# Optimization experiments

Hardware: AMD Instinct MI355X
Metric: run time of the kernel (lower is better)

Reference implementation:

```python
import jax, jax.numpy as jnp
from jax import lax
import numpy as np

GAMMA = 0.25  # bottleneck commitment-loss weight (bn.gamma)
B, Q, N = 8, 64, 8192
K = 512       # n_quant_vecs (codebook size)
C = 256       # n_classes (mu-law quantization levels)


def setup_inputs() -> dict:
    key = jax.random.key(0)
    k1, k2, k3, k4 = jax.random.split(key, 4)
    ze = jax.random.normal(k1, (B, Q, N), dtype=jnp.float32)
    emb = jax.random.normal(k2, (K, Q), dtype=jnp.float32)
    quant_pred = jax.random.normal(k3, (B, C, N), dtype=jnp.float32)
    target_wav = jax.random.randint(k4, (B, N), 0, C, dtype=jnp.int64)
    return {"ze": ze, "emb": emb, "quant_pred": quant_pred, "target_wav": target_wav}


def reference(ze, emb, quant_pred, target_wav):
    # --- VQ codebook nearest-neighbor squared L2 distance ---
    # Original materializes (B,K,Q,N) diff; we use the expansion
    # ||z-e||^2 = ||z||^2 + ||e||^2 - 2 z.e to avoid the huge intermediate.
    ze2 = jnp.sum(ze * ze, axis=1)                       # (B,N)
    emb2 = jnp.sum(emb * emb, axis=1)                    # (K,)
    dots = jnp.einsum('bqn,kq->bkn', ze, emb)            # (B,K,N)
    d = ze2[:, None, :] + emb2[None, :, None] - 2.0 * dots  # (B,K,N)
    kmin = jnp.argmin(lax.stop_gradient(d), axis=1)      # (B,N)
    e_sel = emb[kmin]                                    # (B,N,Q) selected codewords
    ze_t = jnp.transpose(ze, (0, 2, 1))                  # (B,N,Q)

    # l2 loss: sg(ze) vs emb  -> gradient flows to codebook only
    l2_loss = jnp.sum((lax.stop_gradient(ze_t) - e_sel) ** 2, axis=-1)       # (B,N)
    # commitment loss: bn.min_dist uses sg(emb) -> gradient flows to ze only
    com_loss = GAMMA * jnp.sum((ze_t - lax.stop_gradient(e_sel)) ** 2, axis=-1)  # (B,N)

    # --- reconstruction CE: log-softmax over class dim + gather target ---
    log_pred = jax.nn.log_softmax(quant_pred, axis=1)    # (B,C,N)
    lp_t = jnp.take_along_axis(log_pred, target_wav[:, None, :], axis=1)[:, 0, :]  # (B,N)
    rec_loss = -lp_t

    total_loss = rec_loss.sum() + l2_loss.sum() + com_loss.sum()
    return total_loss
```

## Files before the change

### kernel.cpp

```cpp
#include <hip/hip_runtime.h>
#include <math.h>

#define GAMMA 0.25f
constexpr int B_ = 8, Q_ = 64, N_ = 8192, K_ = 512, C_ = 256;

typedef __attribute__((ext_vector_type(8))) short bf16x8;
typedef __attribute__((ext_vector_type(4))) short short4v;
typedef __attribute__((ext_vector_type(4))) float f32x4;

static __device__ inline short f2bf(float x) {
    union { float f; unsigned u; } v; v.f = x;
    unsigned r = (v.u + 0x7fffu + ((v.u >> 16) & 1u)) >> 16;
    return (short)r;
}
static __device__ inline float bf2f(short h) {
    union { unsigned u; float f; } v; v.u = ((unsigned)(unsigned short)h) << 16;
    return v.f;
}

__global__ __launch_bounds__(256) void prep_kernel(const float* __restrict__ emb,
                                                   short* __restrict__ embB,
                                                   float* __restrict__ e2g)
{
    const int r = blockIdx.x * 256 + threadIdx.x;
    if (r >= K_) return;
    const float4* src = (const float4*)(emb + r * Q_);
    short4v* dst = (short4v*)(embB + r * Q_);
    float s = 0.f;
    #pragma unroll
    for (int i = 0; i < 16; ++i) {
        const float4 v = src[i];
        short4v h;
        h[0] = f2bf(v.x); h[1] = f2bf(v.y); h[2] = f2bf(v.z); h[3] = f2bf(v.w);
        dst[i] = h;
        #pragma unroll
        for (int j = 0; j < 4; ++j) { const float a = bf2f(h[j]); s = fmaf(a, a, s); }
    }
    e2g[r] = s;
}

__global__ __launch_bounds__(256) void ce_kernel(const float* __restrict__ qp,
                                                 const int* __restrict__ tgt,
                                                 float* __restrict__ cePart)
{
    __shared__ f32x4 parts[32];
    const int tid  = threadIdx.x;
    const int lane = tid & 63;
    const int w    = tid >> 6;
    const int g    = lane & 7;
    const int c0   = lane >> 3;

    const int base = blockIdx.x * 32;
    const int b    = base >> 13;
    const int n0   = base & (N_ - 1);
    const float* qpb = qp + (size_t)b * C_ * N_;
    const float* qpn = qpb + n0 + g * 4;
    const int cbase  = w * 64 + c0 * 8;

    float4 v[8];
    #pragma unroll
    for (int j = 0; j < 8; ++j)
        v[j] = *(const float4*)(qpn + (size_t)(cbase + j) * N_);

    float xts[4] = {0.f, 0.f, 0.f, 0.f};
    if ((w == 0) && (lane < 8)) {
        #pragma unroll
        for (int j = 0; j < 4; ++j) {
            const int t = tgt[base + lane * 4 + j];
            xts[j] = qpb[(size_t)t * N_ + n0 + lane * 4 + j];
        }
    }

    f32x4 acc = {0.f, 0.f, 0.f, 0.f};
    #pragma unroll
    for (int j = 0; j < 8; ++j) {
        acc[0] += __expf(v[j].x); acc[1] += __expf(v[j].y);
        acc[2] += __expf(v[j].z); acc[3] += __expf(v[j].w);
    }
    #pragma unroll
    for (int r = 0; r < 4; ++r) {
        acc[r] += __shfl_xor(acc[r], 8, 64);
        acc[r] += __shfl_xor(acc[r], 16, 64);
        acc[r] += __shfl_xor(acc[r], 32, 64);
    }
    if (c0 == 0) parts[w * 8 + g] = acc;
    __syncthreads();

    if (w == 0) {
        float loss = 0.f;
        if (lane < 8) {
            const f32x4 tot = (parts[lane] + parts[8 + lane]) +
                              (parts[16 + lane] + parts[24 + lane]);
            #pragma unroll
            for (int j = 0; j < 4; ++j) loss += __logf(tot[j]) - xts[j];
        }
        loss += __shfl_down(loss, 4, 64);
        loss += __shfl_down(loss, 2, 64);
        loss += __shfl_down(loss, 1, 64);
        if (lane == 0) cePart[blockIdx.x] = loss;
    }
}

__global__ __launch_bounds__(256) void vq_kernel(const float* __restrict__ ze,
                                                 const short* __restrict__ embB,
                                                 const float* __restrict__ e2g,
                                                 float* __restrict__ vqPart)
{
    __shared__ f32x4 sh4[(64 * 68 + 256) / 4];
    float* smem = (float*)sh4;
    float* minb = smem + 64 * 68;

    const int tid  = threadIdx.x;
    const int lane = tid & 63;
    const int w    = tid >> 6;
    const int n16  = lane & 15;
    const int quad = lane >> 4;

    const int base = blockIdx.x * 64;
    const int b    = base >> 13;
    const int n0   = base & (N_ - 1);
    const float* zb = ze + (size_t)b * Q_ * N_;

    const int q  = tid >> 2;
    const int pt = tid & 3;
    const float* zq = zb + (size_t)q * N_ + n0 + pt * 4;
    float4 st[4];
    #pragma unroll
    for (int i = 0; i < 4; ++i)
        st[i] = *(const float4*)(zq + i * 16);

    const short* bb = embB + (w * 128 + n16) * Q_ + quad * 8;
    bf16x8 Bv[8][2];
    float  e2v[8];
    #pragma unroll
    for (int t = 0; t < 8; ++t) {
        Bv[t][0] = *(const bf16x8*)(bb + t * 16 * Q_);
        Bv[t][1] = *(const bf16x8*)(bb + t * 16 * Q_ + 32);
        e2v[t]   = e2g[w * 128 + t * 16 + n16];
    }

    #pragma unroll
    for (int i = 0; i < 4; ++i) {
        const int nn = i * 16 + pt * 4;
        smem[(nn + 0) * 68 + q] = st[i].x;
        smem[(nn + 1) * 68 + q] = st[i].y;
        smem[(nn + 2) * 68 + q] = st[i].z;
        smem[(nn + 3) * 68 + q] = st[i].w;
    }
    __syncthreads();

    bf16x8 afrag[4][2];
    float zsq = 0.f;
    #pragma unroll
    for (int u = 0; u < 4; ++u) {
        #pragma unroll
        for (int s = 0; s < 2; ++s) {
            const float* bse = smem + (u * 16 + n16) * 68 + s * 32 + quad * 8;
            const f32x4 x0 = *(const f32x4*)(bse);
            const f32x4 x1 = *(const f32x4*)(bse + 4);
            #pragma unroll
            for (int j = 0; j < 4; ++j) {
                zsq = fmaf(x0[j], x0[j], zsq);
                afrag[u][s][j] = f2bf(-2.f * x0[j]);
            }
            #pragma unroll
            for (int j = 0; j < 4; ++j) {
                zsq = fmaf(x1[j], x1[j], zsq);
                afrag[u][s][4 + j] = f2bf(-2.f * x1[j]);
            }
        }
    }

    f32x4 best[4];
    #pragma unroll
    for (int u = 0; u < 4; ++u) best[u] = (f32x4){1e30f, 1e30f, 1e30f, 1e30f};

    #pragma unroll
    for (int t = 0; t < 8; ++t) {
        const f32x4 ce2 = {e2v[t], e2v[t], e2v[t], e2v[t]};
        #pragma unroll
        for (int u = 0; u < 4; ++u) {
            f32x4 a = __builtin_amdgcn_mfma_f32_16x16x32_bf16(afrag[u][0], Bv[t][0], ce2, 0, 0, 0);
            a       = __builtin_amdgcn_mfma_f32_16x16x32_bf16(afrag[u][1], Bv[t][1], a,   0, 0, 0);
            #pragma unroll
            for (int r = 0; r < 4; ++r) best[u][r] = fminf(best[u][r], a[r]);
        }
    }

    #pragma unroll
    for (int m = 1; m < 16; m <<= 1) {
        #pragma unroll
        for (int u = 0; u < 4; ++u) {
            #pragma unroll
            for (int r = 0; r < 4; ++r)
                best[u][r] = fminf(best[u][r], __shfl_xor(best[u][r], m, 64));
        }
    }
    if (n16 == 0) {
        #pragma unroll
        for (int u = 0; u < 4; ++u) {
            #pragma unroll
            for (int r = 0; r < 4; ++r)
                minb[w * 64 + u * 16 + quad * 4 + r] = best[u][r];
        }
    }
    __syncthreads();

    if (w == 0) {
        const float mn = fminf(fminf(minb[lane], minb[64 + lane]),
                               fminf(minb[128 + lane], minb[192 + lane]));
        float val = 1.25f * (mn + zsq);
        #pragma unroll
        for (int off = 32; off > 0; off >>= 1) val += __shfl_down(val, off, 64);
        if (lane == 0) vqPart[blockIdx.x] = val;
    }
}

__global__ __launch_bounds__(256) void reduce_kernel(const float* __restrict__ cePart,
                                                     const float* __restrict__ vqPart,
                                                     float* __restrict__ out)
{
    __shared__ float sm[4];
    const int tid = threadIdx.x;
    float s = 0.f;
    #pragma unroll
    for (int i = 0; i < 8; ++i) s += cePart[tid + i * 256];
    #pragma unroll
    for (int i = 0; i < 4; ++i) s += vqPart[tid + i * 256];
    #pragma unroll
    for (int off = 32; off > 0; off >>= 1) s += __shfl_down(s, off, 64);
    if ((tid & 63) == 0) sm[tid >> 6] = s;
    __syncthreads();
    if (tid == 0) out[0] = (sm[0] + sm[1]) + (sm[2] + sm[3]);
}

extern "C" void kernel_launch(void* const* d_in, const int* in_sizes, int n_in,
                              void* d_out, int out_size, void* d_ws, size_t ws_size,
                              hipStream_t stream) {
    const float* ze  = (const float*)d_in[0];
    const float* emb = (const float*)d_in[1];
    const float* qp  = (const float*)d_in[2];
    const int*   tgt = (const int*)d_in[3];
    float* out = (float*)d_out;

    short* embB   = (short*)d_ws;
    float* e2g    = (float*)((char*)d_ws + 65536);
    float* cePart = (float*)((char*)d_ws + 65536 + 2048);
    float* vqPart = (float*)((char*)d_ws + 65536 + 2048 + 8192);

    ce_kernel<<<2048, 256, 0, stream>>>(qp, tgt, cePart);
    prep_kernel<<<2, 256, 0, stream>>>(emb, embB, e2g);
    vq_kernel<<<1024, 256, 0, stream>>>(ze, embB, e2g, vqPart);
    reduce_kernel<<<1, 256, 0, stream>>>(cePart, vqPart, out);
}
```

Baseline: 124.5 us.

## Merge CE and VQ kernels into one interleaved launch

Combines the cross-entropy and VQ nearest-codeword kernels into a single 3072-block launch, where every third block runs VQ work and the rest run CE work. This removes one kernel launch and lets the memory-bound CE blocks overlap with the MFMA-heavy VQ blocks on the same CUs. The cost is that every block now reserves the larger VQ shared-memory footprint and the register pressure of the heavier branch, which can lower occupancy for the CE blocks.

```diff
diff --git a/kernel.cpp b/kernel.cpp
--- a/kernel.cpp
+++ b/kernel.cpp
@@ -39,180 +39,180 @@
     e2g[r] = s;
 }
 
-__global__ __launch_bounds__(256) void ce_kernel(const float* __restrict__ qp,
-                                                 const int* __restrict__ tgt,
-                                                 float* __restrict__ cePart)
+__global__ __launch_bounds__(256) void mega_kernel(
+    const float* __restrict__ ze, const float* __restrict__ qp,
+    const int* __restrict__ tgt, const short* __restrict__ embB,
+    const float* __restrict__ e2g,
+    float* __restrict__ cePart, float* __restrict__ vqPart)
 {
-    __shared__ f32x4 parts[32];
+    __shared__ f32x4 sh4[(64 * 68 + 256) / 4];
+    const int bid  = blockIdx.x;
     const int tid  = threadIdx.x;
     const int lane = tid & 63;
     const int w    = tid >> 6;
-    const int g    = lane & 7;
-    const int c0   = lane >> 3;
-
-    const int base = blockIdx.x * 32;
-    const int b    = base >> 13;
-    const int n0   = base & (N_ - 1);
-    const float* qpb = qp + (size_t)b * C_ * N_;
-    const float* qpn = qpb + n0 + g * 4;
-    const int cbase  = w * 64 + c0 * 8;
-
-    float4 v[8];
-    #pragma unroll
-    for (int j = 0; j < 8; ++j)
-        v[j] = *(const float4*)(qpn + (size_t)(cbase + j) * N_);
-
-    float xts[4] = {0.f, 0.f, 0.f, 0.f};
-    if ((w == 0) && (lane < 8)) {
-        #pragma unroll
-        for (int j = 0; j < 4; ++j) {
-            const int t = tgt[base + lane * 4 + j];
-            xts[j] = qpb[(size_t)t * N_ + n0 + lane * 4 + j];
-        }
-    }
-
-    f32x4 acc = {0.f, 0.f, 0.f, 0.f};
-    #pragma unroll
-    for (int j = 0; j < 8; ++j) {
-        acc[0] += __expf(v[j].x); acc[1] += __expf(v[j].y);
-        acc[2] += __expf(v[j].z); acc[3] += __expf(v[j].w);
-    }
-    #pragma unroll
-    for (int r = 0; r < 4; ++r) {
-        acc[r] += __shfl_xor(acc[r], 8, 64);
-        acc[r] += __shfl_xor(acc[r], 16, 64);
-        acc[r] += __shfl_xor(acc[r], 32, 64);
-    }
-    if (c0 == 0) parts[w * 8 + g] = acc;
-    __syncthreads();
-
-    if (w == 0) {
-        float loss = 0.f;
-        if (lane < 8) {
-            const f32x4 tot = (parts[lane] + parts[8 + lane]) +
-                              (parts[16 + lane] + parts[24 + lane]);
-            #pragma unroll
-            for (int j = 0; j < 4; ++j) loss += __logf(tot[j]) - xts[j];
-        }
-        loss += __shfl_down(loss, 4, 64);
-        loss += __shfl_down(loss, 2, 64);
-        loss += __shfl_down(loss, 1, 64);
-        if (lane == 0) cePart[blockIdx.x] = loss;
-    }
-}
-
-__global__ __launch_bounds__(256) void vq_kernel(const float* __restrict__ ze,
-                                                 const short* __restrict__ embB,
-                                                 const float* __restrict__ e2g,
-                                                 float* __restrict__ vqPart)
-{
-    __shared__ f32x4 sh4[(64 * 68 + 256) / 4];
-    float* smem = (float*)sh4;
-    float* minb = smem + 64 * 68;
-
-    const int tid  = threadIdx.x;
-    const int lane = tid & 63;
-    const int w    = tid >> 6;
-    const int n16  = lane & 15;
-    const int quad = lane >> 4;
-
-    const int base = blockIdx.x * 64;
-    const int b    = base >> 13;
-    const int n0   = base & (N_ - 1);
-    const float* zb = ze + (size_t)b * Q_ * N_;
-
-    const int q  = tid >> 2;
-    const int pt = tid & 3;
-    const float* zq = zb + (size_t)q * N_ + n0 + pt * 4;
-    float4 st[4];
-    #pragma unroll
-    for (int i = 0; i < 4; ++i)
-        st[i] = *(const float4*)(zq + i * 16);
-
-    const short* bb = embB + (w * 128 + n16) * Q_ + quad * 8;
-    bf16x8 Bv[8][2];
-    float  e2v[8];
-    #pragma unroll
-    for (int t = 0; t < 8; ++t) {
-        Bv[t][0] = *(const bf16x8*)(bb + t * 16 * Q_);
-        Bv[t][1] = *(const bf16x8*)(bb + t * 16 * Q_ + 32);
-        e2v[t]   = e2g[w * 128 + t * 16 + n16];
-    }
-
-    #pragma unroll
-    for (int i = 0; i < 4; ++i) {
-        const int nn = i * 16 + pt * 4;
-        smem[(nn + 0) * 68 + q] = st[i].x;
-        smem[(nn + 1) * 68 + q] = st[i].y;
-        smem[(nn + 2) * 68 + q] = st[i].z;
-        smem[(nn + 3) * 68 + q] = st[i].w;
-    }
-    __syncthreads();
-
-    bf16x8 afrag[4][2];
-    float zsq = 0.f;
-    #pragma unroll
-    for (int u = 0; u < 4; ++u) {
-        #pragma unroll
-        for (int s = 0; s < 2; ++s) {
-            const float* bse = smem + (u * 16 + n16) * 68 + s * 32 + quad * 8;
-            const f32x4 x0 = *(const f32x4*)(bse);
-            const f32x4 x1 = *(const f32x4*)(bse + 4);
+
+    if (bid % 3 != 0) {
+        const int cbid = bid - bid / 3 - 1;
+        f32x4* parts = sh4;
+
+        const int g    = lane & 7;
+        const int c0   = lane >> 3;
+
+        const int base = cbid * 32;
+        const int b    = base >> 13;
+        const int n0   = base & (N_ - 1);
+        const float* qpb = qp + (size_t)b * C_ * N_;
+        const float* qpn = qpb + n0 + g * 4;
+        const int cbase  = w * 64 + c0 * 8;
+
+        float4 v[8];
+        #pragma unroll
+        for (int j = 0; j < 8; ++j)
+            v[j] = *(const float4*)(qpn + (size_t)(cbase + j) * N_);
+
+        float xts[4] = {0.f, 0.f, 0.f, 0.f};
+        if ((w == 0) && (lane < 8)) {
             #pragma unroll
             for (int j = 0; j < 4; ++j) {
-                zsq = fmaf(x0[j], x0[j], zsq);
-                afrag[u][s][j] = f2bf(-2.f * x0[j]);
-            }
-            #pragma unroll
-            for (int j = 0; j < 4; ++j) {
-                zsq = fmaf(x1[j], x1[j], zsq);
-                afrag[u][s][4 + j] = f2bf(-2.f * x1[j]);
-            }
-        }
-    }
-
-    f32x4 best[4];
-    #pragma unroll
-    for (int u = 0; u < 4; ++u) best[u] = (f32x4){1e30f, 1e30f, 1e30f, 1e30f};
-
-    #pragma unroll
-    for (int t = 0; t < 8; ++t) {
-        const f32x4 ce2 = {e2v[t], e2v[t], e2v[t], e2v[t]};
+                const int t = tgt[base + lane * 4 + j];
+                xts[j] = qpb[(size_t)t * N_ + n0 + lane * 4 + j];
+            }
+        }
+
+        f32x4 acc = {0.f, 0.f, 0.f, 0.f};
+        #pragma unroll
+        for (int j = 0; j < 8; ++j) {
+            acc[0] += __expf(v[j].x); acc[1] += __expf(v[j].y);
+            acc[2] += __expf(v[j].z); acc[3] += __expf(v[j].w);
+        }
+        #pragma unroll
+        for (int r = 0; r < 4; ++r) {
+            acc[r] += __shfl_xor(acc[r], 8, 64);
+            acc[r] += __shfl_xor(acc[r], 16, 64);
+            acc[r] += __shfl_xor(acc[r], 32, 64);
+        }
+        if (c0 == 0) parts[w * 8 + g] = acc;
+        __syncthreads();
+
+        if (w == 0) {
+            float loss = 0.f;
+            if (lane < 8) {
+                const f32x4 tot = (parts[lane] + parts[8 + lane]) +
+                                  (parts[16 + lane] + parts[24 + lane]);
+                #pragma unroll
+                for (int j = 0; j < 4; ++j) loss += __logf(tot[j]) - xts[j];
+            }
+            loss += __shfl_down(loss, 4, 64);
+            loss += __shfl_down(loss, 2, 64);
+            loss += __shfl_down(loss, 1, 64);
+            if (lane == 0) cePart[cbid] = loss;
+        }
+    } else {
+        const int vbid = bid / 3;
+        float* smem = (float*)sh4;
+        float* minb = smem + 64 * 68;
+
+        const int n16  = lane & 15;
+        const int quad = lane >> 4;
+
+        const int base = vbid * 64;
+        const int b    = base >> 13;
+        const int n0   = base & (N_ - 1);
+        const float* zb = ze + (size_t)b * Q_ * N_;
+
+        const int q  = tid >> 2;
+        const int pt = tid & 3;
+        const float* zq = zb + (size_t)q * N_ + n0 + pt * 4;
+        float4 st[4];
+        #pragma unroll
+        for (int i = 0; i < 4; ++i)
+            st[i] = *(const float4*)(zq + i * 16);
+
+        const short* bb = embB + (w * 128 + n16) * Q_ + quad * 8;
+        bf16x8 Bv[8][2];
+        float  e2v[8];
+        #pragma unroll
+        for (int t = 0; t < 8; ++t) {
+            Bv[t][0] = *(const bf16x8*)(bb + t * 16 * Q_);
+            Bv[t][1] = *(const bf16x8*)(bb + t * 16 * Q_ + 32);
+            e2v[t]   = e2g[w * 128 + t * 16 + n16];
+        }
+
+        #pragma unroll
+        for (int i = 0; i < 4; ++i) {
+            const int nn = i * 16 + pt * 4;
+            smem[(nn + 0) * 68 + q] = st[i].x;
+            smem[(nn + 1) * 68 + q] = st[i].y;
+            smem[(nn + 2) * 68 + q] = st[i].z;
+            smem[(nn + 3) * 68 + q] = st[i].w;
+        }
+        __syncthreads();
+
+        bf16x8 afrag[4][2];
+        float zsq = 0.f;
         #pragma unroll
         for (int u = 0; u < 4; ++u) {
-            f32x4 a = __builtin_amdgcn_mfma_f32_16x16x32_bf16(afrag[u][0], Bv[t][0], ce2, 0, 0, 0);
-            a       = __builtin_amdgcn_mfma_f32_16x16x32_bf16(afrag[u][1], Bv[t][1], a,   0, 0, 0);
-            #pragma unroll
-            for (int r = 0; r < 4; ++r) best[u][r] = fminf(best[u][r], a[r]);
-        }
-    }
-
-    #pragma unroll
-    for (int m = 1; m < 16; m <<= 1) {
-        #pragma unroll
-        for (int u = 0; u < 4; ++u) {
-            #pragma unroll
-            for (int r = 0; r < 4; ++r)
-                best[u][r] = fminf(best[u][r], __shfl_xor(best[u][r], m, 64));
-        }
-    }
-    if (n16 == 0) {
-        #pragma unroll
-        for (int u = 0; u < 4; ++u) {
-            #pragma unroll
-            for (int r = 0; r < 4; ++r)
-                minb[w * 64 + u * 16 + quad * 4 + r] = best[u][r];
-        }
-    }
-    __syncthreads();
-
-    if (w == 0) {
-        const float mn = fminf(fminf(minb[lane], minb[64 + lane]),
-                               fminf(minb[128 + lane], minb[192 + lane]));
-        float val = 1.25f * (mn + zsq);
-        #pragma unroll
-        for (int off = 32; off > 0; off >>= 1) val += __shfl_down(val, off, 64);
-        if (lane == 0) vqPart[blockIdx.x] = val;
+            #pragma unroll
+            for (int s = 0; s < 2; ++s) {
+                const float* bse = smem + (u * 16 + n16) * 68 + s * 32 + quad * 8;
+                const f32x4 x0 = *(const f32x4*)(bse);
+                const f32x4 x1 = *(const f32x4*)(bse + 4);
+                #pragma unroll
+                for (int j = 0; j < 4; ++j) {
+                    zsq = fmaf(x0[j], x0[j], zsq);
+                    afrag[u][s][j] = f2bf(-2.f * x0[j]);
+                }
+                #pragma unroll
+                for (int j = 0; j < 4; ++j) {
+                    zsq = fmaf(x1[j], x1[j], zsq);
+                    afrag[u][s][4 + j] = f2bf(-2.f * x1[j]);
+                }
+            }
+        }
+
+        f32x4 best[4];
+        #pragma unroll
+        for (int u = 0; u < 4; ++u) best[u] = (f32x4){1e30f, 1e30f, 1e30f, 1e30f};
+
+        #pragma unroll
+        for (int t = 0; t < 8; ++t) {
+            const f32x4 ce2 = {e2v[t], e2v[t], e2v[t], e2v[t]};
+            #pragma unroll
+            for (int u = 0; u < 4; ++u) {
+                f32x4 a = __builtin_amdgcn_mfma_f32_16x16x32_bf16(afrag[u][0], Bv[t][0], ce2, 0, 0, 0);
+                a       = __builtin_amdgcn_mfma_f32_16x16x32_bf16(afrag[u][1], Bv[t][1], a,   0, 0, 0);
+                #pragma unroll
+                for (int r = 0; r < 4; ++r) best[u][r] = fminf(best[u][r], a[r]);
+            }
+        }
+
+        #pragma unroll
+        for (int m = 1; m < 16; m <<= 1) {
+            #pragma unroll
+            for (int u = 0; u < 4; ++u) {
+                #pragma unroll
+                for (int r = 0; r < 4; ++r)
+                    best[u][r] = fminf(best[u][r], __shfl_xor(best[u][r], m, 64));
+            }
+        }
+        if (n16 == 0) {
+            #pragma unroll
+            for (int u = 0; u < 4; ++u) {
+                #pragma unroll
+                for (int r = 0; r < 4; ++r)
+                    minb[w * 64 + u * 16 + quad * 4 + r] = best[u][r];
+            }
+        }
+        __syncthreads();
+
+        if (w == 0) {
+            const float mn = fminf(fminf(minb[lane], minb[64 + lane]),
+                                   fminf(minb[128 + lane], minb[192 + lane]));
+            float val = 1.25f * (mn + zsq);
+            #pragma unroll
+            for (int off = 32; off > 0; off >>= 1) val += __shfl_down(val, off, 64);
+            if (lane == 0) vqPart[vbid] = val;
+        }
     }
 }
 
@@ -248,8 +248,7 @@
     float* cePart = (float*)((char*)d_ws + 65536 + 2048);
     float* vqPart = (float*)((char*)d_ws + 65536 + 2048 + 8192);
 
-    ce_kernel<<<2048, 256, 0, stream>>>(qp, tgt, cePart);
     prep_kernel<<<2, 256, 0, stream>>>(emb, embB, e2g);
-    vq_kernel<<<1024, 256, 0, stream>>>(ze, embB, e2g, vqPart);
+    mega_kernel<<<3072, 256, 0, stream>>>(ze, qp, tgt, embB, e2g, cePart, vqPart);
     reduce_kernel<<<1, 256, 0, stream>>>(cePart, vqPart, out);
 }
```

New measurement: 123.2 us (median of 2 runs). No clear change (-1.0%).
